# Performance work log

Hardware: AMD Instinct MI355X
Metric: run time of the kernel (lower is better)

The kernel has to match this reference:

```python
import jax, jax.numpy as jnp
import numpy as np

E, TOPK, HID, FFN = 8, 2, 1024, 2048  # experts, top_k, hidden K, intermediate N
B, S = 2, 1024


def setup_inputs() -> dict:
    key = jax.random.key(0)
    ks = jax.random.split(key, 7)
    return {
        "x": jax.random.normal(ks[0], (B, S, HID), jnp.float32),
        "router_weight": jax.random.normal(ks[1], (E, HID), jnp.float32) * 0.02,
        "router_bias": jax.random.normal(ks[2], (E,), jnp.float32) * 0.02,
        "w1": jax.random.normal(ks[3], (E, 2 * FFN, HID), jnp.float32) * 0.02,  # [E,2N,K] gate|up
        "w1_bias": jax.random.normal(ks[4], (E, 2 * FFN), jnp.float32) * 0.02,
        "w2": jax.random.normal(ks[5], (E, HID, FFN), jnp.float32) * 0.02,      # [E,K,N]
        "w2_bias": jax.random.normal(ks[6], (E, HID), jnp.float32) * 0.02,
        "top_k": TOPK,
    }


def reference(x, router_weight, router_bias, w1, w1_bias, w2, w2_bias, top_k):
    Bb, Ss, K = x.shape
    xf = x.reshape(-1, K)                                   # [M,K]
    M = xf.shape[0]
    Ne = w1.shape[0]
    # --- route_tokens: softmax over experts, then top-k (megablocks style) ---
    logits = xf @ router_weight.T + router_bias             # [M,E]
    probs = jax.nn.softmax(logits, axis=-1)
    topk_w, topk_ids = jax.lax.top_k(probs, top_k)          # [M,topk]
    # combine weights: scatter top-k probs into dense [M,E]
    comb = jnp.zeros((M, Ne), xf.dtype).at[jnp.arange(M)[:, None], topk_ids].add(topk_w)
    # --- fused experts (dense combine formulation, same math as grouped GEMM) ---
    gu = jnp.einsum('mk,enk->men', xf, w1) + w1_bias[None]  # [M,E,2N]
    Nf = gu.shape[-1] // 2
    gate, up = gu[..., :Nf], gu[..., Nf:]
    h = jax.nn.silu(gate) * up                              # silu_and_mul (SwiGLU)
    down = jnp.einsum('men,ekn->mek', h, w2) + w2_bias[None]  # [M,E,K]
    out = jnp.einsum('mek,me->mk', down, comb)              # weighted combine
    return out.reshape(Bb, Ss, K), topk_w
```

## Files before the change

kernel.cpp:

```cpp
#include <hip/hip_runtime.h>
#include <hip/hip_bf16.h>
#include <math.h>

#define E_    8
#define HID_  1024
#define FFN_  2048
#define M_    2048
#define NP_   (M_*2)

typedef __attribute__((ext_vector_type(8))) short bf16x8;
typedef __attribute__((ext_vector_type(4))) float f32x4;

typedef const __attribute__((address_space(1))) void GVOID;
typedef __attribute__((address_space(3))) void LVOID;

#define VMCNT4 asm volatile("s_waitcnt vmcnt(4)" ::: "memory")
#define VMCNT0 asm volatile("s_waitcnt vmcnt(0)" ::: "memory")

__device__ __forceinline__ short f2bf(float f) {
    union { __hip_bfloat16 b; short s; } u;
    u.b = __float2bfloat16(f);
    return u.s;
}

__global__ __launch_bounds__(256) void cvt_kernel(
    const float* __restrict__ src, __hip_bfloat16* __restrict__ dst, int n4)
{
    int stride = gridDim.x * 256;
    for (int i = blockIdx.x * 256 + threadIdx.x; i < n4; i += stride) {
        float4 v = ((const float4*)src)[i];
        short4 o;
        o.x = f2bf(v.x); o.y = f2bf(v.y); o.z = f2bf(v.z); o.w = f2bf(v.w);
        ((short4*)dst)[i] = o;
    }
}

__global__ __launch_bounds__(64) void router_kernel(
    const float* __restrict__ x, const float* __restrict__ rw,
    const float* __restrict__ rb, int* __restrict__ ids,
    float* __restrict__ wts, int* __restrict__ cnt,
    float* __restrict__ topk_out)
{
    const int m    = blockIdx.x;
    const int lane = threadIdx.x;
    const float4* xm4 = (const float4*)(x + (size_t)m * HID_);

    float4 xv[4];
#pragma unroll
    for (int j = 0; j < 4; ++j) xv[j] = xm4[j*64 + lane];

    float lg[E_];
#pragma unroll
    for (int e = 0; e < E_; ++e) {
        const float4* we4 = (const float4*)(rw + e * HID_);
        float s = 0.f;
#pragma unroll
        for (int j = 0; j < 4; ++j) {
            float4 w = we4[j*64 + lane];
            s = fmaf(xv[j].x, w.x, s);
            s = fmaf(xv[j].y, w.y, s);
            s = fmaf(xv[j].z, w.z, s);
            s = fmaf(xv[j].w, w.w, s);
        }
        lg[e] = s;
    }
#pragma unroll
    for (int off = 32; off; off >>= 1)
#pragma unroll
        for (int e = 0; e < E_; ++e) lg[e] += __shfl_xor(lg[e], off);

    if (lane == 0) {
        float l2[E_], p[E_];
        float mx = -1e30f;
#pragma unroll
        for (int e = 0; e < E_; ++e) { l2[e] = lg[e] + rb[e]; mx = fmaxf(mx, l2[e]); }
        float sum = 0.f;
#pragma unroll
        for (int e = 0; e < E_; ++e) { p[e] = expf(l2[e] - mx); sum += p[e]; }
        float inv = 1.f / sum;
#pragma unroll
        for (int e = 0; e < E_; ++e) p[e] *= inv;

        int   i1 = -1, i2 = -1;
        float v1 = -1e30f, v2 = -1e30f;
#pragma unroll
        for (int e = 0; e < E_; ++e) {
            float pe = p[e];
            if (pe > v1)      { v2 = v1; i2 = i1; v1 = pe; i1 = e; }
            else if (pe > v2) { v2 = pe; i2 = e; }
        }
        ids[2*m]   = i1;  ids[2*m+1]   = i2;
        wts[2*m]   = v1;  wts[2*m+1]   = v2;
        topk_out[2*m]   = v1;
        topk_out[2*m+1] = v2;
        atomicAdd(&cnt[i1], 1);
        atomicAdd(&cnt[i2], 1);
    }
}

__global__ void offsets_kernel(const int* __restrict__ cnt,
                               int* __restrict__ off, int* __restrict__ fill)
{
    if (threadIdx.x == 0 && blockIdx.x == 0) {
        int acc = 0;
        for (int e = 0; e < E_; ++e) { off[e] = acc; fill[e] = acc; acc += cnt[e]; }
    }
}

__global__ __launch_bounds__(256) void scatter_kernel(
    const int* __restrict__ ids, const float* __restrict__ wts,
    int* __restrict__ fill, int* __restrict__ gtok, float* __restrict__ gwt,
    int* __restrict__ pos)
{
    int m = blockIdx.x * 256 + threadIdx.x;
    if (m >= M_) return;
#pragma unroll
    for (int s = 0; s < 2; ++s) {
        int e = ids[2*m + s];
        int p = atomicAdd(&fill[e], 1);
        gtok[p] = m;
        gwt[p]  = wts[2*m + s];
        pos[2*m + s] = p;
    }
}


__global__ __launch_bounds__(256, 3) void gemm1_kernel(
    const __hip_bfloat16* __restrict__ xb, const __hip_bfloat16* __restrict__ w1bf,
    const float* __restrict__ w1b, const int* __restrict__ gtok,
    const int* __restrict__ cnt, const int* __restrict__ off,
    __hip_bfloat16* __restrict__ h)
{
    const int e  = blockIdx.z;
    const int ce = cnt[e];
    const int t0 = blockIdx.y * 128;
    if (t0 >= ce) return;
    const int n0   = blockIdx.x * 64;
    const int base = off[e];
    const __hip_bfloat16* w1e = w1bf + (size_t)e * (2*FFN_) * HID_;

    __shared__ __align__(16) __hip_bfloat16 As[3][128*32];
    __shared__ __align__(16) __hip_bfloat16 Bs[3][128*32];

    const int tid  = threadIdx.x;
    const int lane = tid & 63;
    const int wid  = tid >> 6;
    const int wm   = wid >> 1;
    const int wn   = wid & 1;

    const __hip_bfloat16 *asrc[2], *bsrc[2];
#pragma unroll
    for (int q = 0; q < 2; ++q) {
        int slot = q*256 + tid;
        int r = slot >> 2, p = slot & 3;
        int c = p ^ ((r >> 1) & 3);
        int rr  = min(t0 + r, ce - 1);
        asrc[q] = xb + (size_t)gtok[base + rr] * HID_ + c*8;
        int q2 = r >> 5, s = r & 31;
        int grow = (q2 & 1) ? (FFN_ + n0 + (q2>>1)*32 + s)
                            : (       n0 + (q2>>1)*32 + s);
        bsrc[q] = w1e + (size_t)grow * HID_ + c*8;
    }

    auto STAGE = [&](int b, int k0) {
#pragma unroll
        for (int q = 0; q < 2; ++q)
            __builtin_amdgcn_global_load_lds((GVOID*)(asrc[q] + k0),
                (LVOID*)(&As[b][(q*256 + wid*64)*8]), 16, 0, 0);
#pragma unroll
        for (int q = 0; q < 2; ++q)
            __builtin_amdgcn_global_load_lds((GVOID*)(bsrc[q] + k0),
                (LVOID*)(&Bs[b][(q*256 + wid*64)*8]), 16, 0, 0);
    };

    f32x4 acc[4][4];
#pragma unroll
    for (int m = 0; m < 4; ++m)
#pragma unroll
        for (int n = 0; n < 4; ++n) acc[m][n] = (f32x4){0.f,0.f,0.f,0.f};

    const int cf = lane >> 4;
    auto COMPUTE = [&](int cb) {
        bf16x8 af[4], bfr[4];
#pragma unroll
        for (int m = 0; m < 4; ++m) {
            int r = wm*64 + m*16 + (lane & 15);
            int sw = cf ^ ((r >> 1) & 3);
            af[m] = *(bf16x8*)&As[cb][r*32 + sw*8];
        }
#pragma unroll
        for (int n = 0; n < 4; ++n) {
            int r = wn*64 + n*16 + (lane & 15);
            int sw = cf ^ ((r >> 1) & 3);
            bfr[n] = *(bf16x8*)&Bs[cb][r*32 + sw*8];
        }
        __builtin_amdgcn_s_setprio(1);
#pragma unroll
        for (int m = 0; m < 4; ++m)
#pragma unroll
            for (int n = 0; n < 4; ++n)
                acc[m][n] = __builtin_amdgcn_mfma_f32_16x16x32_bf16(
                    af[m], bfr[n], acc[m][n], 0, 0, 0);
        __builtin_amdgcn_s_setprio(0);
    };

    const int NT = HID_/32;
    STAGE(0, 0);
    STAGE(1, 32);
    VMCNT4;
    __builtin_amdgcn_s_barrier();

    int cb = 0;
    for (int t = 0; t < NT-2; ++t) {
        int sb = cb + 2; if (sb >= 3) sb -= 3;
        STAGE(sb, (t+2)*32);
        COMPUTE(cb);
        VMCNT4;
        __builtin_amdgcn_s_barrier();
        if (++cb == 3) cb = 0;
    }
    COMPUTE(cb);
    VMCNT0;
    __builtin_amdgcn_s_barrier();
    if (++cb == 3) cb = 0;
    COMPUTE(cb);

    const float* w1be = w1b + e*2*FFN_;
#pragma unroll
    for (int n = 0; n < 2; ++n) {
        int col = n0 + wn*32 + n*16 + (lane & 15);
        float bg = w1be[col];
        float bu = w1be[FFN_ + col];
#pragma unroll
        for (int m = 0; m < 4; ++m) {
            int rb2 = t0 + wm*64 + m*16 + (lane >> 4)*4;
#pragma unroll
            for (int i = 0; i < 4; ++i) {
                int t = rb2 + i;
                if (t < ce) {
                    float g = acc[m][n][i]   + bg;
                    float u = acc[m][n+2][i] + bu;
                    float hv = (g / (1.f + __expf(-g))) * u;
                    h[(size_t)(base + t)*FFN_ + col] = __float2bfloat16(hv);
                }
            }
        }
    }
}

__global__ __launch_bounds__(256, 3) void gemm2_kernel(
    const __hip_bfloat16* __restrict__ h, const __hip_bfloat16* __restrict__ w2bf,
    const float* __restrict__ w2b, const float* __restrict__ gwt,
    const int* __restrict__ cnt, const int* __restrict__ off,
    float* __restrict__ dpair)
{
    const int e  = blockIdx.z & 7;
    const int ks = blockIdx.z >> 3;
    const int ce = cnt[e];
    const int t0 = blockIdx.y * 128;
    if (t0 >= ce) return;
    const int n0    = blockIdx.x * 128;
    const int base  = off[e];
    const int kbase = ks * (FFN_/2);
    const __hip_bfloat16* w2e = w2bf + (size_t)e * HID_ * FFN_;

    __shared__ __align__(16) __hip_bfloat16 As[3][128*32];
    __shared__ __align__(16) __hip_bfloat16 Bs[3][128*32];

    const int tid  = threadIdx.x;
    const int lane = tid & 63;
    const int wid  = tid >> 6;
    const int wm   = wid >> 1;
    const int wn   = wid & 1;

    const __hip_bfloat16 *asrc[2], *bsrc[2];
#pragma unroll
    for (int q = 0; q < 2; ++q) {
        int slot = q*256 + tid;
        int r = slot >> 2, p = slot & 3;
        int c = p ^ ((r >> 1) & 3);
        int rr = min(t0 + r, ce - 1);
        asrc[q] = h   + (size_t)(base + rr) * FFN_ + kbase + c*8;
        bsrc[q] = w2e + (size_t)(n0 + r)    * FFN_ + kbase + c*8;
    }

    auto STAGE = [&](int b, int k0) {
#pragma unroll
        for (int q = 0; q < 2; ++q)
            __builtin_amdgcn_global_load_lds((GVOID*)(asrc[q] + k0),
                (LVOID*)(&As[b][(q*256 + wid*64)*8]), 16, 0, 0);
#pragma unroll
        for (int q = 0; q < 2; ++q)
            __builtin_amdgcn_global_load_lds((GVOID*)(bsrc[q] + k0),
                (LVOID*)(&Bs[b][(q*256 + wid*64)*8]), 16, 0, 0);
    };

    f32x4 acc[4][4];
#pragma unroll
    for (int m = 0; m < 4; ++m)
#pragma unroll
        for (int n = 0; n < 4; ++n) acc[m][n] = (f32x4){0.f,0.f,0.f,0.f};

    const int cf = lane >> 4;
    auto COMPUTE = [&](int cb) {
        bf16x8 af[4], bfr[4];
#pragma unroll
        for (int m = 0; m < 4; ++m) {
            int r = wm*64 + m*16 + (lane & 15);
            int sw = cf ^ ((r >> 1) & 3);
            af[m] = *(bf16x8*)&As[cb][r*32 + sw*8];
        }
#pragma unroll
        for (int n = 0; n < 4; ++n) {
            int r = wn*64 + n*16 + (lane & 15);
            int sw = cf ^ ((r >> 1) & 3);
            bfr[n] = *(bf16x8*)&Bs[cb][r*32 + sw*8];
        }
        __builtin_amdgcn_s_setprio(1);
#pragma unroll
        for (int m = 0; m < 4; ++m)
#pragma unroll
            for (int n = 0; n < 4; ++n)
                acc[m][n] = __builtin_amdgcn_mfma_f32_16x16x32_bf16(
                    af[m], bfr[n], acc[m][n], 0, 0, 0);
        __builtin_amdgcn_s_setprio(0);
    };

    const int NT = (FFN_/2)/32;
    STAGE(0, 0);
    STAGE(1, 32);
    VMCNT4;
    __builtin_amdgcn_s_barrier();

    int cb = 0;
    for (int t = 0; t < NT-2; ++t) {
        int sb = cb + 2; if (sb >= 3) sb -= 3;
        STAGE(sb, (t+2)*32);
        COMPUTE(cb);
        VMCNT4;
        __builtin_amdgcn_s_barrier();
        if (++cb == 3) cb = 0;
    }
    COMPUTE(cb);
    VMCNT0;
    __builtin_amdgcn_s_barrier();
    if (++cb == 3) cb = 0;
    COMPUTE(cb);

    const float* w2be = w2b + e*HID_;
    float* dpk = dpair + (size_t)ks * NP_ * HID_;
#pragma unroll
    for (int n = 0; n < 4; ++n) {
        int col = n0 + wn*64 + n*16 + (lane & 15);
        float bias = (ks == 0) ? w2be[col] : 0.f;
#pragma unroll
        for (int m = 0; m < 4; ++m) {
            int rb2 = t0 + wm*64 + m*16 + (lane >> 4)*4;
#pragma unroll
            for (int i = 0; i < 4; ++i) {
                int t = rb2 + i;
                if (t < ce) {
                    int p   = base + t;
                    float w = gwt[p];
                    dpk[(size_t)p*HID_ + col] = w * (acc[m][n][i] + bias);
                }
            }
        }
    }
}

__global__ __launch_bounds__(256) void combine_kernel(
    const float* __restrict__ dpair, const int* __restrict__ pos,
    float* __restrict__ out)
{
    int idx = blockIdx.x * 256 + threadIdx.x;
    int m   = idx >> 8;
    int c4  = (idx & 255) * 4;
    int p0 = pos[2*m], p1 = pos[2*m+1];
    const float* d0 = dpair;
    const float* d1 = dpair + (size_t)NP_ * HID_;
    float4 a0 = *(const float4*)(d0 + (size_t)p0*HID_ + c4);
    float4 a1 = *(const float4*)(d1 + (size_t)p0*HID_ + c4);
    float4 b0 = *(const float4*)(d0 + (size_t)p1*HID_ + c4);
    float4 b1 = *(const float4*)(d1 + (size_t)p1*HID_ + c4);
    float4 o = make_float4((a0.x+a1.x)+(b0.x+b1.x), (a0.y+a1.y)+(b0.y+b1.y),
                           (a0.z+a1.z)+(b0.z+b1.z), (a0.w+a1.w)+(b0.w+b1.w));
    *(float4*)(out + (size_t)m*HID_ + c4) = o;
}

__global__ __launch_bounds__(256) void gemm1_rs_kernel(
    const __hip_bfloat16* __restrict__ xb, const float* __restrict__ w1,
    const float* __restrict__ w1b, const int* __restrict__ gtok,
    const int* __restrict__ cnt, const int* __restrict__ off,
    __hip_bfloat16* __restrict__ h)
{
    const int e  = blockIdx.z;
    const int ce = cnt[e];
    const int t0 = blockIdx.y * 128;
    if (t0 >= ce) return;
    const int n0   = blockIdx.x * 64;
    const int base = off[e];
    const float* w1e = w1 + (size_t)e * (2*FFN_) * HID_;

    __shared__ __align__(16) __hip_bfloat16 As[128*64];
    __shared__ __align__(16) __hip_bfloat16 Bs[128*64];

    const int tid  = threadIdx.x;
    const int lane = tid & 63;
    const int wid  = tid >> 6;
    const int wm   = wid >> 1;
    const int wn   = wid & 1;

    const __hip_bfloat16* asrc[4];
#pragma unroll
    for (int q = 0; q < 4; ++q) {
        int slot = q*256 + tid;
        int r = slot >> 3, p = slot & 7;
        int rr  = min(t0 + r, ce - 1);
        int tok = gtok[base + rr];
        int c = p ^ (r & 7);
        asrc[q] = xb + (size_t)tok * HID_ + c*8;
    }

    const int brow = tid >> 1;
    const int hk   = tid & 1;
    const int q2 = brow >> 5, s = brow & 31;
    const int grow = (q2 & 1) ? (FFN_ + n0 + (q2>>1)*32 + s)
                              : (       n0 + (q2>>1)*32 + s);
    const float* bsrc = w1e + (size_t)grow * HID_ + hk*32;

    f32x4 acc[4][4];
#pragma unroll
    for (int m = 0; m < 4; ++m)
#pragma unroll
        for (int n = 0; n < 4; ++n) acc[m][n] = (f32x4){0.f,0.f,0.f,0.f};

    float4 breg[8];
#pragma unroll
    for (int j = 0; j < 8; ++j) breg[j] = *(const float4*)(bsrc + j*4);

    for (int k0 = 0; k0 < HID_; k0 += 64) {
#pragma unroll
        for (int q = 0; q < 4; ++q) {
            __builtin_amdgcn_global_load_lds(
                (GVOID*)(asrc[q] + k0),
                (LVOID*)(&As[(q*256 + wid*64)*8]), 16, 0, 0);
        }
#pragma unroll
        for (int cc = 0; cc < 4; ++cc) {
            union { bf16x8 v; short s8[8]; } u;
            const float* f0 = (const float*)&breg[2*cc];
#pragma unroll
            for (int j = 0; j < 8; ++j) u.s8[j] = f2bf(f0[j]);
            int c = hk*4 + cc, p = c ^ (brow & 7);
            *(bf16x8*)&Bs[brow*64 + p*8] = u.v;
        }
        __syncthreads();

        if (k0 + 64 < HID_) {
#pragma unroll
            for (int j = 0; j < 8; ++j) breg[j] = *(const float4*)(bsrc + (k0+64) + j*4);
        }

        bf16x8 af[4][2], bfr[4][2];
#pragma unroll
        for (int m = 0; m < 4; ++m)
#pragma unroll
            for (int kk = 0; kk < 2; ++kk) {
                int r = wm*64 + m*16 + (lane & 15);
                int c = kk*4 + (lane >> 4), p = c ^ (r & 7);
                af[m][kk] = *(bf16x8*)&As[r*64 + p*8];
            }
#pragma unroll
        for (int n = 0; n < 4; ++n)
#pragma unroll
            for (int kk = 0; kk < 2; ++kk) {
                int r = wn*64 + n*16 + (lane & 15);
                int c = kk*4 + (lane >> 4), p = c ^ (r & 7);
                bfr[n][kk] = *(bf16x8*)&Bs[r*64 + p*8];
            }
#pragma unroll
        for (int kk = 0; kk < 2; ++kk)
#pragma unroll
            for (int m = 0; m < 4; ++m)
#pragma unroll
                for (int n = 0; n < 4; ++n)
                    acc[m][n] = __builtin_amdgcn_mfma_f32_16x16x32_bf16(
                        af[m][kk], bfr[n][kk], acc[m][n], 0, 0, 0);
        __syncthreads();
    }

    const float* w1be = w1b + e*2*FFN_;
#pragma unroll
    for (int n = 0; n < 2; ++n) {
        int col = n0 + wn*32 + n*16 + (lane & 15);
        float bg = w1be[col];
        float bu = w1be[FFN_ + col];
#pragma unroll
        for (int m = 0; m < 4; ++m) {
            int rb2 = t0 + wm*64 + m*16 + (lane >> 4)*4;
#pragma unroll
            for (int i = 0; i < 4; ++i) {
                int t = rb2 + i;
                if (t < ce) {
                    float g = acc[m][n][i]   + bg;
                    float u = acc[m][n+2][i] + bu;
                    float hv = (g / (1.f + __expf(-g))) * u;
                    h[(size_t)(base + t)*FFN_ + col] = __float2bfloat16(hv);
                }
            }
        }
    }
}

__global__ __launch_bounds__(256) void gemm2_rs_kernel(
    const __hip_bfloat16* __restrict__ h, const float* __restrict__ w2,
    const float* __restrict__ w2b, const int* __restrict__ gtok,
    const float* __restrict__ gwt, const int* __restrict__ cnt,
    const int* __restrict__ off, float* __restrict__ out)
{
    const int e  = blockIdx.z;
    const int ce = cnt[e];
    const int t0 = blockIdx.y * 128;
    if (t0 >= ce) return;
    const int n0   = blockIdx.x * 128;
    const int base = off[e];
    const float* w2e = w2 + (size_t)e * HID_ * FFN_;

    __shared__ __align__(16) __hip_bfloat16 As[128*64];
    __shared__ __align__(16) __hip_bfloat16 Bs[128*64];

    const int tid  = threadIdx.x;
    const int lane = tid & 63;
    const int wid  = tid >> 6;
    const int wm   = wid >> 1;
    const int wn   = wid & 1;

    const __hip_bfloat16* asrc[4];
#pragma unroll
    for (int q = 0; q < 4; ++q) {
        int slot = q*256 + tid;
        int r = slot >> 3, p = slot & 7;
        int rr = min(t0 + r, ce - 1);
        int c = p ^ (r & 7);
        asrc[q] = h + (size_t)(base + rr) * FFN_ + c*8;
    }

    const int brow = tid >> 1;
    const int hk   = tid & 1;
    const float* bsrc = w2e + (size_t)(n0 + brow) * FFN_ + hk*32;

    f32x4 acc[4][4];
#pragma unroll
    for (int m = 0; m < 4; ++m)
#pragma unroll
        for (int n = 0; n < 4; ++n) acc[m][n] = (f32x4){0.f,0.f,0.f,0.f};

    float4 breg[8];
#pragma unroll
    for (int j = 0; j < 8; ++j) breg[j] = *(const float4*)(bsrc + j*4);

    for (int k0 = 0; k0 < FFN_; k0 += 64) {
#pragma unroll
        for (int q = 0; q < 4; ++q) {
            __builtin_amdgcn_global_load_lds(
                (GVOID*)(asrc[q] + k0),
                (LVOID*)(&As[(q*256 + wid*64)*8]), 16, 0, 0);
        }
#pragma unroll
        for (int cc = 0; cc < 4; ++cc) {
            union { bf16x8 v; short s8[8]; } u;
            const float* f0 = (const float*)&breg[2*cc];
#pragma unroll
            for (int j = 0; j < 8; ++j) u.s8[j] = f2bf(f0[j]);
            int c = hk*4 + cc, p = c ^ (brow & 7);
            *(bf16x8*)&Bs[brow*64 + p*8] = u.v;
        }
        __syncthreads();

        if (k0 + 64 < FFN_) {
#pragma unroll
            for (int j = 0; j < 8; ++j) breg[j] = *(const float4*)(bsrc + (k0+64) + j*4);
        }

        bf16x8 af[4][2], bfr[4][2];
#pragma unroll
        for (int m = 0; m < 4; ++m)
#pragma unroll
            for (int kk = 0; kk < 2; ++kk) {
                int r = wm*64 + m*16 + (lane & 15);
                int c = kk*4 + (lane >> 4), p = c ^ (r & 7);
                af[m][kk] = *(bf16x8*)&As[r*64 + p*8];
            }
#pragma unroll
        for (int n = 0; n < 4; ++n)
#pragma unroll
            for (int kk = 0; kk < 2; ++kk) {
                int r = wn*64 + n*16 + (lane & 15);
                int c = kk*4 + (lane >> 4), p = c ^ (r & 7);
                bfr[n][kk] = *(bf16x8*)&Bs[r*64 + p*8];
            }
#pragma unroll
        for (int kk = 0; kk < 2; ++kk)
#pragma unroll
            for (int m = 0; m < 4; ++m)
#pragma unroll
                for (int n = 0; n < 4; ++n)
                    acc[m][n] = __builtin_amdgcn_mfma_f32_16x16x32_bf16(
                        af[m][kk], bfr[n][kk], acc[m][n], 0, 0, 0);
        __syncthreads();
    }

    const float* w2be = w2b + e*HID_;
#pragma unroll
    for (int n = 0; n < 4; ++n) {
        int col = n0 + wn*64 + n*16 + (lane & 15);
        float bias = w2be[col];
#pragma unroll
        for (int m = 0; m < 4; ++m) {
            int rb2 = t0 + wm*64 + m*16 + (lane >> 4)*4;
#pragma unroll
            for (int i = 0; i < 4; ++i) {
                int t = rb2 + i;
                if (t < ce) {
                    int p   = base + t;
                    float w = gwt[p];
                    atomicAdd(&out[(size_t)gtok[p]*HID_ + col], w * (acc[m][n][i] + bias));
                }
            }
        }
    }
}

extern "C" void kernel_launch(void* const* d_in, const int* in_sizes, int n_in,
                              void* d_out, int out_size, void* d_ws, size_t ws_size,
                              hipStream_t stream)
{
    const float* x   = (const float*)d_in[0];
    const float* rw  = (const float*)d_in[1];
    const float* rb  = (const float*)d_in[2];
    const float* w1  = (const float*)d_in[3];
    const float* w1b = (const float*)d_in[4];
    const float* w2  = (const float*)d_in[5];
    const float* w2b = (const float*)d_in[6];

    float* out      = (float*)d_out;
    float* topk_out = out + (size_t)M_ * HID_;

    char*  ws   = (char*)d_ws;
    int*   ids  = (int*)  (ws);
    float* wts  = (float*)(ws + 16384);
    int*   gtok = (int*)  (ws + 32768);
    float* gwt  = (float*)(ws + 49152);
    int*   cnt  = (int*)  (ws + 65536);
    int*   off  = (int*)  (ws + 65536 + 128);
    int*   fill = (int*)  (ws + 65536 + 256);
    int*   pos  = (int*)  (ws + 98304);

    const size_t MB = 1024*1024;
    __hip_bfloat16* xb    = (__hip_bfloat16*)(ws + 131072);
    __hip_bfloat16* h     = (__hip_bfloat16*)(ws + 131072 + 4*MB);
    float*          dpair = (float*)         (ws + 131072 + 20*MB);
    __hip_bfloat16* w1bf  = (__hip_bfloat16*)(ws + 131072 + 52*MB);
    __hip_bfloat16* w2bf  = (__hip_bfloat16*)(ws + 131072 + 116*MB);
    const bool tier2 = (ws_size >= 131072 + 148*MB);

    hipMemsetAsync(cnt, 0, E_ * sizeof(int), stream);

    cvt_kernel<<<2048, 256, 0, stream>>>(x, xb, (M_*HID_)/4);
    router_kernel<<<M_, 64, 0, stream>>>(x, rw, rb, ids, wts, cnt, topk_out);
    offsets_kernel<<<1, 64, 0, stream>>>(cnt, off, fill);
    scatter_kernel<<<M_/256, 256, 0, stream>>>(ids, wts, fill, gtok, gwt, pos);

    if (tier2) {
        cvt_kernel<<<4096, 256, 0, stream>>>(w1, w1bf, (E_*2*FFN_*HID_)/4);
        cvt_kernel<<<4096, 256, 0, stream>>>(w2, w2bf, (E_*HID_*FFN_)/4);

        dim3 g1(FFN_/64, M_/128, E_);
        gemm1_kernel<<<g1, 256, 0, stream>>>(xb, w1bf, w1b, gtok, cnt, off, h);

        dim3 g2(HID_/128, M_/128, 2*E_);
        gemm2_kernel<<<g2, 256, 0, stream>>>(h, w2bf, w2b, gwt, cnt, off, dpair);

        combine_kernel<<<(M_*HID_)/(256*4), 256, 0, stream>>>(dpair, pos, out);
    } else {
        hipMemsetAsync(out, 0, (size_t)M_ * HID_ * sizeof(float), stream);

        dim3 g1(FFN_/64, M_/128, E_);
        gemm1_rs_kernel<<<g1, 256, 0, stream>>>(xb, w1, w1b, gtok, cnt, off, h);

        dim3 g2(HID_/128, M_/128, E_);
        gemm2_rs_kernel<<<g2, 256, 0, stream>>>(h, w2, w2b, gtok, gwt, cnt, off, out);
    }
}
```

Before: 252.2 us.

## Enlarge GEMM token tiles to 256, fuse x conversion into router, merge weight casts

Both grouped GEMMs now cover 256 token rows per block instead of 128. Each warp holds an 8x4 accumulator tile and loads A fragments per row inside the MFMA loop, so weight tiles are reused across more tokens and weight traffic drops. To fit the larger tiles, occupancy is lowered to 2 blocks per SM and the vmcnt wait is raised to match the extra in-flight loads. The x-to-bf16 cast is folded into the router kernel, and the two weight casts share one kernel, which removes launches. The risks are more register pressure and more idle rows for experts whose token counts fit the larger tile poorly.

```diff
diff --git a/kernel.cpp b/kernel.cpp
--- a/kernel.cpp
+++ b/kernel.cpp
@@ -14,7 +14,7 @@
 typedef const __attribute__((address_space(1))) void GVOID;
 typedef __attribute__((address_space(3))) void LVOID;
 
-#define VMCNT4 asm volatile("s_waitcnt vmcnt(4)" ::: "memory")
+#define VMCNT6 asm volatile("s_waitcnt vmcnt(6)" ::: "memory")
 #define VMCNT0 asm volatile("s_waitcnt vmcnt(0)" ::: "memory")
 
 __device__ __forceinline__ short f2bf(float f) {
@@ -23,15 +23,21 @@
     return u.s;
 }
 
-__global__ __launch_bounds__(256) void cvt_kernel(
-    const float* __restrict__ src, __hip_bfloat16* __restrict__ dst, int n4)
-{
+__global__ __launch_bounds__(256) void cvt_w_kernel(
+    const float* __restrict__ w1, const float* __restrict__ w2,
+    __hip_bfloat16* __restrict__ w1bf, __hip_bfloat16* __restrict__ w2bf)
+{
+    const int n1 = (E_*2*FFN_*HID_)/4;
+    const int n2 = (E_*HID_*FFN_)/4;
     int stride = gridDim.x * 256;
-    for (int i = blockIdx.x * 256 + threadIdx.x; i < n4; i += stride) {
-        float4 v = ((const float4*)src)[i];
+    for (int i = blockIdx.x * 256 + threadIdx.x; i < n1 + n2; i += stride) {
+        float4 v;
+        if (i < n1) v = ((const float4*)w1)[i];
+        else        v = ((const float4*)w2)[i - n1];
         short4 o;
         o.x = f2bf(v.x); o.y = f2bf(v.y); o.z = f2bf(v.z); o.w = f2bf(v.w);
-        ((short4*)dst)[i] = o;
+        if (i < n1) ((short4*)w1bf)[i] = o;
+        else        ((short4*)w2bf)[i - n1] = o;
     }
 }
 
@@ -39,7 +45,7 @@
     const float* __restrict__ x, const float* __restrict__ rw,
     const float* __restrict__ rb, int* __restrict__ ids,
     float* __restrict__ wts, int* __restrict__ cnt,
-    float* __restrict__ topk_out)
+    float* __restrict__ topk_out, __hip_bfloat16* __restrict__ xb)
 {
     const int m    = blockIdx.x;
     const int lane = threadIdx.x;
@@ -48,6 +54,15 @@
     float4 xv[4];
 #pragma unroll
     for (int j = 0; j < 4; ++j) xv[j] = xm4[j*64 + lane];
+
+    short4* xbr = (short4*)(xb + (size_t)m * HID_);
+#pragma unroll
+    for (int j = 0; j < 4; ++j) {
+        short4 o;
+        o.x = f2bf(xv[j].x); o.y = f2bf(xv[j].y);
+        o.z = f2bf(xv[j].z); o.w = f2bf(xv[j].w);
+        xbr[j*64 + lane] = o;
+    }
 
     float lg[E_];
 #pragma unroll
@@ -125,7 +140,7 @@
 }
 
 
-__global__ __launch_bounds__(256, 3) void gemm1_kernel(
+__global__ __launch_bounds__(256, 2) void gemm1_kernel(
     const __hip_bfloat16* __restrict__ xb, const __hip_bfloat16* __restrict__ w1bf,
     const float* __restrict__ w1b, const int* __restrict__ gtok,
     const int* __restrict__ cnt, const int* __restrict__ off,
@@ -133,13 +148,13 @@
 {
     const int e  = blockIdx.z;
     const int ce = cnt[e];
-    const int t0 = blockIdx.y * 128;
+    const int t0 = blockIdx.y * 256;
     if (t0 >= ce) return;
     const int n0   = blockIdx.x * 64;
     const int base = off[e];
     const __hip_bfloat16* w1e = w1bf + (size_t)e * (2*FFN_) * HID_;
 
-    __shared__ __align__(16) __hip_bfloat16 As[3][128*32];
+    __shared__ __align__(16) __hip_bfloat16 As[3][256*32];
     __shared__ __align__(16) __hip_bfloat16 Bs[3][128*32];
 
     const int tid  = threadIdx.x;
@@ -148,14 +163,20 @@
     const int wm   = wid >> 1;
     const int wn   = wid & 1;
 
-    const __hip_bfloat16 *asrc[2], *bsrc[2];
-#pragma unroll
-    for (int q = 0; q < 2; ++q) {
+    const __hip_bfloat16 *asrc[4], *bsrc[2];
+#pragma unroll
+    for (int q = 0; q < 4; ++q) {
         int slot = q*256 + tid;
         int r = slot >> 2, p = slot & 3;
         int c = p ^ ((r >> 1) & 3);
         int rr  = min(t0 + r, ce - 1);
         asrc[q] = xb + (size_t)gtok[base + rr] * HID_ + c*8;
+    }
+#pragma unroll
+    for (int q = 0; q < 2; ++q) {
+        int slot = q*256 + tid;
+        int r = slot >> 2, p = slot & 3;
+        int c = p ^ ((r >> 1) & 3);
         int q2 = r >> 5, s = r & 31;
         int grow = (q2 & 1) ? (FFN_ + n0 + (q2>>1)*32 + s)
                             : (       n0 + (q2>>1)*32 + s);
@@ -164,7 +185,7 @@
 
     auto STAGE = [&](int b, int k0) {
 #pragma unroll
-        for (int q = 0; q < 2; ++q)
+        for (int q = 0; q < 4; ++q)
             __builtin_amdgcn_global_load_lds((GVOID*)(asrc[q] + k0),
                 (LVOID*)(&As[b][(q*256 + wid*64)*8]), 16, 0, 0);
 #pragma unroll
@@ -173,21 +194,15 @@
                 (LVOID*)(&Bs[b][(q*256 + wid*64)*8]), 16, 0, 0);
     };
 
-    f32x4 acc[4][4];
-#pragma unroll
-    for (int m = 0; m < 4; ++m)
+    f32x4 acc[8][4];
+#pragma unroll
+    for (int m = 0; m < 8; ++m)
 #pragma unroll
         for (int n = 0; n < 4; ++n) acc[m][n] = (f32x4){0.f,0.f,0.f,0.f};
 
     const int cf = lane >> 4;
     auto COMPUTE = [&](int cb) {
-        bf16x8 af[4], bfr[4];
-#pragma unroll
-        for (int m = 0; m < 4; ++m) {
-            int r = wm*64 + m*16 + (lane & 15);
-            int sw = cf ^ ((r >> 1) & 3);
-            af[m] = *(bf16x8*)&As[cb][r*32 + sw*8];
-        }
+        bf16x8 bfr[4];
 #pragma unroll
         for (int n = 0; n < 4; ++n) {
             int r = wn*64 + n*16 + (lane & 15);
@@ -196,18 +211,22 @@
         }
         __builtin_amdgcn_s_setprio(1);
 #pragma unroll
-        for (int m = 0; m < 4; ++m)
+        for (int m = 0; m < 8; ++m) {
+            int r = wm*128 + m*16 + (lane & 15);
+            int sw = cf ^ ((r >> 1) & 3);
+            bf16x8 af = *(bf16x8*)&As[cb][r*32 + sw*8];
 #pragma unroll
             for (int n = 0; n < 4; ++n)
                 acc[m][n] = __builtin_amdgcn_mfma_f32_16x16x32_bf16(
-                    af[m], bfr[n], acc[m][n], 0, 0, 0);
+                    af, bfr[n], acc[m][n], 0, 0, 0);
+        }
         __builtin_amdgcn_s_setprio(0);
     };
 
     const int NT = HID_/32;
     STAGE(0, 0);
     STAGE(1, 32);
-    VMCNT4;
+    VMCNT6;
     __builtin_amdgcn_s_barrier();
 
     int cb = 0;
@@ -215,7 +234,7 @@
         int sb = cb + 2; if (sb >= 3) sb -= 3;
         STAGE(sb, (t+2)*32);
         COMPUTE(cb);
-        VMCNT4;
+        VMCNT6;
         __builtin_amdgcn_s_barrier();
         if (++cb == 3) cb = 0;
     }
@@ -232,8 +251,8 @@
         float bg = w1be[col];
         float bu = w1be[FFN_ + col];
 #pragma unroll
-        for (int m = 0; m < 4; ++m) {
-            int rb2 = t0 + wm*64 + m*16 + (lane >> 4)*4;
+        for (int m = 0; m < 8; ++m) {
+            int rb2 = t0 + wm*128 + m*16 + (lane >> 4)*4;
 #pragma unroll
             for (int i = 0; i < 4; ++i) {
                 int t = rb2 + i;
@@ -248,7 +267,7 @@
     }
 }
 
-__global__ __launch_bounds__(256, 3) void gemm2_kernel(
+__global__ __launch_bounds__(256, 2) void gemm2_kernel(
     const __hip_bfloat16* __restrict__ h, const __hip_bfloat16* __restrict__ w2bf,
     const float* __restrict__ w2b, const float* __restrict__ gwt,
     const int* __restrict__ cnt, const int* __restrict__ off,
@@ -257,14 +276,14 @@
     const int e  = blockIdx.z & 7;
     const int ks = blockIdx.z >> 3;
     const int ce = cnt[e];
-    const int t0 = blockIdx.y * 128;
+    const int t0 = blockIdx.y * 256;
     if (t0 >= ce) return;
     const int n0    = blockIdx.x * 128;
     const int base  = off[e];
     const int kbase = ks * (FFN_/2);
     const __hip_bfloat16* w2e = w2bf + (size_t)e * HID_ * FFN_;
 
-    __shared__ __align__(16) __hip_bfloat16 As[3][128*32];
+    __shared__ __align__(16) __hip_bfloat16 As[3][256*32];
     __shared__ __align__(16) __hip_bfloat16 Bs[3][128*32];
 
     const int tid  = threadIdx.x;
@@ -273,20 +292,26 @@
     const int wm   = wid >> 1;
     const int wn   = wid & 1;
 
-    const __hip_bfloat16 *asrc[2], *bsrc[2];
+    const __hip_bfloat16 *asrc[4], *bsrc[2];
+#pragma unroll
+    for (int q = 0; q < 4; ++q) {
+        int slot = q*256 + tid;
+        int r = slot >> 2, p = slot & 3;
+        int c = p ^ ((r >> 1) & 3);
+        int rr = min(t0 + r, ce - 1);
+        asrc[q] = h + (size_t)(base + rr) * FFN_ + kbase + c*8;
+    }
 #pragma unroll
     for (int q = 0; q < 2; ++q) {
         int slot = q*256 + tid;
         int r = slot >> 2, p = slot & 3;
         int c = p ^ ((r >> 1) & 3);
-        int rr = min(t0 + r, ce - 1);
-        asrc[q] = h   + (size_t)(base + rr) * FFN_ + kbase + c*8;
-        bsrc[q] = w2e + (size_t)(n0 + r)    * FFN_ + kbase + c*8;
+        bsrc[q] = w2e + (size_t)(n0 + r) * FFN_ + kbase + c*8;
     }
 
     auto STAGE = [&](int b, int k0) {
 #pragma unroll
-        for (int q = 0; q < 2; ++q)
+        for (int q = 0; q < 4; ++q)
             __builtin_amdgcn_global_load_lds((GVOID*)(asrc[q] + k0),
                 (LVOID*)(&As[b][(q*256 + wid*64)*8]), 16, 0, 0);
 #pragma unroll
@@ -295,21 +320,15 @@
                 (LVOID*)(&Bs[b][(q*256 + wid*64)*8]), 16, 0, 0);
     };
 
-    f32x4 acc[4][4];
-#pragma unroll
-    for (int m = 0; m < 4; ++m)
+    f32x4 acc[8][4];
+#pragma unroll
+    for (int m = 0; m < 8; ++m)
 #pragma unroll
         for (int n = 0; n < 4; ++n) acc[m][n] = (f32x4){0.f,0.f,0.f,0.f};
 
     const int cf = lane >> 4;
     auto COMPUTE = [&](int cb) {
-        bf16x8 af[4], bfr[4];
-#pragma unroll
-        for (int m = 0; m < 4; ++m) {
-            int r = wm*64 + m*16 + (lane & 15);
-            int sw = cf ^ ((r >> 1) & 3);
-            af[m] = *(bf16x8*)&As[cb][r*32 + sw*8];
-        }
+        bf16x8 bfr[4];
 #pragma unroll
         for (int n = 0; n < 4; ++n) {
             int r = wn*64 + n*16 + (lane & 15);
@@ -318,18 +337,22 @@
         }
         __builtin_amdgcn_s_setprio(1);
 #pragma unroll
-        for (int m = 0; m < 4; ++m)
+        for (int m = 0; m < 8; ++m) {
+            int r = wm*128 + m*16 + (lane & 15);
+            int sw = cf ^ ((r >> 1) & 3);
+            bf16x8 af = *(bf16x8*)&As[cb][r*32 + sw*8];
 #pragma unroll
             for (int n = 0; n < 4; ++n)
                 acc[m][n] = __builtin_amdgcn_mfma_f32_16x16x32_bf16(
-                    af[m], bfr[n], acc[m][n], 0, 0, 0);
+                    af, bfr[n], acc[m][n], 0, 0, 0);
+        }
         __builtin_amdgcn_s_setprio(0);
     };
 
     const int NT = (FFN_/2)/32;
     STAGE(0, 0);
     STAGE(1, 32);
-    VMCNT4;
+    VMCNT6;
     __builtin_amdgcn_s_barrier();
 
     int cb = 0;
@@ -337,7 +360,7 @@
         int sb = cb + 2; if (sb >= 3) sb -= 3;
         STAGE(sb, (t+2)*32);
         COMPUTE(cb);
-        VMCNT4;
+        VMCNT6;
         __builtin_amdgcn_s_barrier();
         if (++cb == 3) cb = 0;
     }
@@ -354,8 +377,8 @@
         int col = n0 + wn*64 + n*16 + (lane & 15);
         float bias = (ks == 0) ? w2be[col] : 0.f;
 #pragma unroll
-        for (int m = 0; m < 4; ++m) {
-            int rb2 = t0 + wm*64 + m*16 + (lane >> 4)*4;
+        for (int m = 0; m < 8; ++m) {
+            int rb2 = t0 + wm*128 + m*16 + (lane >> 4)*4;
 #pragma unroll
             for (int i = 0; i < 4; ++i) {
                 int t = rb2 + i;
@@ -667,19 +690,17 @@
 
     hipMemsetAsync(cnt, 0, E_ * sizeof(int), stream);
 
-    cvt_kernel<<<2048, 256, 0, stream>>>(x, xb, (M_*HID_)/4);
-    router_kernel<<<M_, 64, 0, stream>>>(x, rw, rb, ids, wts, cnt, topk_out);
+    router_kernel<<<M_, 64, 0, stream>>>(x, rw, rb, ids, wts, cnt, topk_out, xb);
     offsets_kernel<<<1, 64, 0, stream>>>(cnt, off, fill);
     scatter_kernel<<<M_/256, 256, 0, stream>>>(ids, wts, fill, gtok, gwt, pos);
 
     if (tier2) {
-        cvt_kernel<<<4096, 256, 0, stream>>>(w1, w1bf, (E_*2*FFN_*HID_)/4);
-        cvt_kernel<<<4096, 256, 0, stream>>>(w2, w2bf, (E_*HID_*FFN_)/4);
-
-        dim3 g1(FFN_/64, M_/128, E_);
+        cvt_w_kernel<<<4096, 256, 0, stream>>>(w1, w2, w1bf, w2bf);
+
+        dim3 g1(FFN_/64, M_/256, E_);
         gemm1_kernel<<<g1, 256, 0, stream>>>(xb, w1bf, w1b, gtok, cnt, off, h);
 
-        dim3 g2(HID_/128, M_/128, 2*E_);
+        dim3 g2(HID_/128, M_/256, 2*E_);
         gemm2_kernel<<<g2, 256, 0, stream>>>(h, w2bf, w2b, gwt, cnt, off, dpair);
 
         combine_kernel<<<(M_*HID_)/(256*4), 256, 0, stream>>>(dpair, pos, out);
```

Measured after the change: 285.2 us. 13.1% more time.
